# Optimization experiments

Hardware: AMD Instinct MI355X
Metric: run time of the kernel (lower is better)

Reference implementation:

```python
import jax, jax.numpy as jnp
import numpy as np

N_NODES = 30000
N_EDGES = 100000
N_GRAPHS = 256
HEADS = 4
NEG_SLOPE = 0.2


def _xavier(key, shape):
    fan_in, fan_out = shape[-2], shape[-1]
    limit = (6.0 / (fan_in + fan_out)) ** 0.5
    return jax.random.uniform(key, shape, jnp.float32, -limit, limit)


def setup_inputs() -> dict:
    key = jax.random.key(0)
    ks = jax.random.split(key, 12)
    x = jax.random.normal(ks[0], (N_NODES, 78), jnp.float32)
    edge_index = jax.random.randint(ks[1], (2, N_EDGES), 0, N_NODES, jnp.int64)
    # sorted graph ids covering all N_GRAPHS segments
    batch = (jnp.arange(N_NODES, dtype=jnp.int64) * N_GRAPHS) // N_NODES
    # conv1: 78 -> 78 per head
    W1 = _xavier(ks[2], (78, HEADS * 78))
    att1 = _xavier(ks[3], (1, HEADS, 2 * 78))
    b1 = jnp.zeros((HEADS * 78,), jnp.float32)
    # conv2: 312 -> 156 per head
    W2 = _xavier(ks[4], (312, HEADS * 156))
    att2 = _xavier(ks[5], (1, HEADS, 2 * 156))
    b2 = jnp.zeros((HEADS * 156,), jnp.float32)
    # conv3: 624 -> 312 per head
    W3 = _xavier(ks[6], (624, HEADS * 312))
    att3 = _xavier(ks[7], (1, HEADS, 2 * 312))
    b3 = jnp.zeros((HEADS * 312,), jnp.float32)
    Wg1 = _xavier(ks[8], (1248, 1024)); bg1 = jnp.zeros((1024,), jnp.float32)
    Wg2 = _xavier(ks[9], (1024, 128)); bg2 = jnp.zeros((128,), jnp.float32)
    Wo = _xavier(ks[10], (128, 1)); bo = jnp.zeros((1,), jnp.float32)
    return {"x": x, "edge_index": edge_index, "batch": batch,
            "W1": W1, "att1": att1, "b1": b1,
            "W2": W2, "att2": att2, "b2": b2,
            "W3": W3, "att3": att3, "b3": b3,
            "Wg1": Wg1, "bg1": bg1, "Wg2": Wg2, "bg2": bg2,
            "Wo": Wo, "bo": bo}


def gat_conv(x, edge_index, W, att, b, out_ch):
    # x: [N, in]; W: [in, heads*out]; att: [1, heads, 2*out]
    n = x.shape[0]
    xh = (x @ W).reshape(n, HEADS, out_ch)            # [N, H, C]
    src, dst = edge_index[0], edge_index[1]           # x_j = src, x_i = dst (target)
    xi = xh[dst]                                      # [E, H, C]
    xj = xh[src]                                      # [E, H, C]
    cat = jnp.concatenate([xi, xj], axis=-1)          # [E, H, 2C]
    alpha = (cat * att).sum(-1)                       # [E, H]
    alpha = jax.nn.leaky_relu(alpha, NEG_SLOPE)
    # NOTE: softmax over heads (dim=1), as in the original code
    alpha = jax.nn.softmax(alpha, axis=1)
    msg = xj * alpha[..., None]                       # [E, H, C]
    agg = jax.ops.segment_sum(msg, dst, num_segments=n)  # [N, H, C]
    return agg.reshape(n, HEADS * out_ch) + b


def reference(x, edge_index, batch, W1, att1, b1, W2, att2, b2, W3, att3, b3,
              Wg1, bg1, Wg2, bg2, Wo, bo):
    h = jax.nn.relu(gat_conv(x, edge_index, W1, att1, b1, 78))
    h = jax.nn.relu(gat_conv(h, edge_index, W2, att2, b2, 156))
    h = jax.nn.relu(gat_conv(h, edge_index, W3, att3, b3, 312))
    # global max pool per graph
    g = jax.ops.segment_max(h, batch, num_segments=N_GRAPHS)  # [G, 1248]
    g = jax.nn.relu(g @ Wg1 + bg1)
    g = g @ Wg2 + bg2
    return g @ Wo + bo  # [G, 1]
```

## Files before the change

kernel.cpp:

```cpp
#include <hip/hip_runtime.h>
#include <hip/hip_bf16.h>

#define N_NODES 30000
#define N_GRAPHS 256
#define HEADS 4
#define NBLK_SCAN ((N_NODES + 255) / 256)

typedef __attribute__((ext_vector_type(8))) short short8;
typedef __attribute__((ext_vector_type(4))) float f32x4;
typedef __attribute__((ext_vector_type(4))) unsigned short ushort4_t;
typedef unsigned short ushort_t;

__device__ __forceinline__ ushort_t f2bf(float v) {
    __hip_bfloat16 h = __float2bfloat16(v);
    return *reinterpret_cast<ushort_t*>(&h);
}
__device__ __forceinline__ float bf2f(ushort_t u) {
    __hip_bfloat16 h;
    *reinterpret_cast<ushort_t*>(&h) = u;
    return __bfloat162float(h);
}
__device__ __forceinline__ int ld_idx(const void* p, long i, int is64) {
    return is64 ? (int)((const long long*)p)[i] : ((const int*)p)[i];
}
__device__ __forceinline__ int clampi(int v, int hi) {
    return v < 0 ? 0 : (v > hi ? hi : v);
}

__global__ void detect_fmt(const void* ei, const void* batch, int E, int* flags)
{
    __shared__ int okE, okB;
    if (threadIdx.x == 0) { okE = 1; okB = 1; }
    __syncthreads();
    const long long* e64 = (const long long*)ei;
    const long long* b64 = (const long long*)batch;
    const int nbslot = N_NODES / 2;
    for (int i = threadIdx.x; i < 2048; i += 256) {
        long ei_idx = (long)i * E / 2048;
        long long v = e64[ei_idx];
        if (v < 0 || v >= N_NODES) okE = 0;
        long b_idx = (long)i * nbslot / 2048;
        long long b = b64[b_idx];
        if (b < 0 || b >= N_GRAPHS) okB = 0;
    }
    __syncthreads();
    if (threadIdx.x == 0) { flags[0] = okE; flags[1] = okB; }
}

__global__ void init_zero(int* __restrict__ indeg, int* __restrict__ gcnt)
{
    int i = blockIdx.x * 256 + threadIdx.x;
    if (i < N_NODES) indeg[i] = 0;
    if (i < N_GRAPHS) gcnt[i] = 0;
}

__global__ void zero_pads(ushort_t* __restrict__ H1b, ushort_t* __restrict__ H2b)
{
    int n = blockIdx.x * blockDim.x + threadIdx.x;
    if (n >= N_NODES) return;
    ushort4_t z = {0, 0, 0, 0};
    *(ushort4_t*)&H1b[(long)n * 320 + 312] = z;
    *(ushort4_t*)&H1b[(long)n * 320 + 316] = z;
#pragma unroll
    for (int q = 0; q < 4; ++q)
        *(ushort4_t*)&H2b[(long)n * 640 + 624 + q * 4] = z;
}

__global__ void csr_hist(const void* ei, const void* batch, const int* __restrict__ flags,
                         int* __restrict__ indeg, int* __restrict__ gcnt, int E)
{
    int i = blockIdx.x * blockDim.x + threadIdx.x;
    if (i < E) {
        int d = clampi(ld_idx(ei, (long)E + i, flags[0]), N_NODES - 1);
        atomicAdd(&indeg[d], 1);
    }
    if (i < N_NODES) {
        int g = clampi(ld_idx(batch, i, flags[1]), N_GRAPHS - 1);
        atomicAdd(&gcnt[g], 1);
    }
}

__global__ __launch_bounds__(256) void scan_a(const int* __restrict__ indeg,
                                              int* __restrict__ locpre,
                                              int* __restrict__ bsum)
{
    __shared__ int ps[256];
    const int t = threadIdx.x;
    const int i = blockIdx.x * 256 + t;
    int v = (i < N_NODES) ? indeg[i] : 0;
    ps[t] = v;
    __syncthreads();
    for (int d = 1; d < 256; d <<= 1) {
        int u = (t >= d) ? ps[t - d] : 0;
        __syncthreads();
        ps[t] += u;
        __syncthreads();
    }
    if (i < N_NODES) locpre[i] = ps[t] - v;
    if (t == 255) bsum[blockIdx.x] = ps[255];
}

__global__ __launch_bounds__(256) void scan_b(const int* __restrict__ bsum,
                                              int* __restrict__ bbase,
                                              int* __restrict__ totE,
                                              const int* __restrict__ gcnt,
                                              int* __restrict__ gstart)
{
    __shared__ int ps[256];
    const int t = threadIdx.x;
    int v = (t < NBLK_SCAN) ? bsum[t] : 0;
    ps[t] = v;
    __syncthreads();
    for (int d = 1; d < 256; d <<= 1) {
        int u = (t >= d) ? ps[t - d] : 0;
        __syncthreads();
        ps[t] += u;
        __syncthreads();
    }
    if (t < NBLK_SCAN) bbase[t] = ps[t] - v;
    if (t == 255) totE[0] = ps[255];
    __syncthreads();
    int gv = gcnt[t];
    ps[t] = gv;
    __syncthreads();
    for (int d = 1; d < 256; d <<= 1) {
        int u = (t >= d) ? ps[t - d] : 0;
        __syncthreads();
        ps[t] += u;
        __syncthreads();
    }
    gstart[t + 1] = ps[t];
    if (t == 0) gstart[0] = 0;
}

__global__ void scan_c(const int* __restrict__ locpre, const int* __restrict__ bbase,
                       const int* __restrict__ totE,
                       int* __restrict__ off, int* __restrict__ cursor)
{
    int i = blockIdx.x * 256 + threadIdx.x;
    if (i < N_NODES) {
        int o = locpre[i] + bbase[blockIdx.x];
        off[i] = o;
        cursor[i] = o;
    }
    if (i == 0) off[N_NODES] = totE[0];
}

__global__ void csr_fill(const void* ei, const int* __restrict__ flags,
                         int* __restrict__ cursor, int* __restrict__ slots,
                         int* __restrict__ srcs, int E)
{
    int i = blockIdx.x * blockDim.x + threadIdx.x;
    if (i >= E) return;
    int is64 = flags[0];
    int d = clampi(ld_idx(ei, (long)E + i, is64), N_NODES - 1);
    int s = clampi(ld_idx(ei, i, is64), N_NODES - 1);
    int p = atomicAdd(&cursor[d], 1);
    slots[p] = i;
    srcs[p] = s;
}

__global__ void conv_pad_bf16(const float* __restrict__ src, ushort_t* __restrict__ dst,
                              int K, int Kp, long M)
{
    long total = M * Kp;
    long stride = (long)gridDim.x * blockDim.x;
    for (long i = (long)blockIdx.x * blockDim.x + threadIdx.x; i < total; i += stride) {
        long n = i / Kp;
        int k = (int)(i - n * Kp);
        dst[i] = (k < K) ? f2bf(src[n * K + k]) : (ushort_t)0;
    }
}

__global__ void prep_weights(const float* __restrict__ W, const float* __restrict__ att,
                             ushort_t* __restrict__ WT, float* __restrict__ Wd,
                             float* __restrict__ Wsv, int K, int Kp, int C, int HC)
{
    int i = blockIdx.x * blockDim.x + threadIdx.x;
    if (blockIdx.y == 0) {
        int nch = Kp >> 3;
        if (i >= HC * nch) return;
        int n = i / nch, c8 = i - n * nch;
#pragma unroll
        for (int e = 0; e < 8; ++e) {
            int k = c8 * 8 + e;
            WT[(long)n * Kp + k] = (k < K) ? f2bf(W[(long)k * HC + n]) : (ushort_t)0;
        }
    } else {
        if (i >= K * HEADS) return;
        int k = i >> 2, h = i & 3;
        const float* wrow = W + (long)k * HC + h * C;
        const float* ad = att + h * 2 * C;
        const float* as = ad + C;
        float s1 = 0.f, s2 = 0.f;
        for (int c = 0; c < C; ++c) { float w = wrow[c]; s1 += w * ad[c]; s2 += w * as[c]; }
        Wd[k * HEADS + h] = s1;
        Wsv[k * HEADS + h] = s2;
    }
}

__global__ __launch_bounds__(256) void node_proj_any(const void* __restrict__ A,
                                                     int lda, int K, int isbf,
                                                     const float* __restrict__ Wd,
                                                     const float* __restrict__ Wsv,
                                                     float* __restrict__ adst,
                                                     float* __restrict__ asrc, int N)
{
    const int wv = threadIdx.x >> 6, lane = threadIdx.x & 63;
    const int n0 = (blockIdx.x * 4 + wv) * 2;
    if (n0 >= N) return;
    const int n1 = min(n0 + 1, N - 1);

    f32x4 sd0 = {0.f, 0.f, 0.f, 0.f}, ss0 = sd0, sd1 = sd0, ss1 = sd0;

    if (isbf) {
        const ushort_t* a0 = (const ushort_t*)A + (long)n0 * lda;
        const ushort_t* a1 = (const ushort_t*)A + (long)n1 * lda;
        for (int k = lane; k < K; k += 64) {
            float v0 = bf2f(a0[k]);
            float v1 = bf2f(a1[k]);
            f32x4 wd = *(const f32x4*)&Wd[k * HEADS];
            f32x4 wsv = *(const f32x4*)&Wsv[k * HEADS];
            sd0 += v0 * wd; ss0 += v0 * wsv;
            sd1 += v1 * wd; ss1 += v1 * wsv;
        }
    } else {
        const float* a0 = (const float*)A + (long)n0 * lda;
        const float* a1 = (const float*)A + (long)n1 * lda;
        for (int k = lane; k < K; k += 64) {
            float v0 = a0[k];
            float v1 = a1[k];
            f32x4 wd = *(const f32x4*)&Wd[k * HEADS];
            f32x4 wsv = *(const f32x4*)&Wsv[k * HEADS];
            sd0 += v0 * wd; ss0 += v0 * wsv;
            sd1 += v1 * wd; ss1 += v1 * wsv;
        }
    }
#pragma unroll
    for (int off = 32; off; off >>= 1) {
#pragma unroll
        for (int h = 0; h < 4; ++h) {
            sd0[h] += __shfl_down(sd0[h], off);
            ss0[h] += __shfl_down(ss0[h], off);
            sd1[h] += __shfl_down(sd1[h], off);
            ss1[h] += __shfl_down(ss1[h], off);
        }
    }
    if (lane == 0) {
        *(f32x4*)&adst[n0 * HEADS] = sd0;
        *(f32x4*)&asrc[n0 * HEADS] = ss0;
        if (n1 != n0) {
            *(f32x4*)&adst[n1 * HEADS] = sd1;
            *(f32x4*)&asrc[n1 * HEADS] = ss1;
        }
    }
}

__global__ void edge_alpha_csr(const int* __restrict__ slots,
                               const void* __restrict__ ei, const int* __restrict__ flags,
                               const float* __restrict__ adst, const float* __restrict__ asrc,
                               float* __restrict__ alphac, int E)
{
    int p = blockIdx.x * blockDim.x + threadIdx.x;
    if (p >= E) return;
    int is64 = flags[0];
    int e = slots[p];
    int s = clampi(ld_idx(ei, e, is64), N_NODES - 1);
    int d = clampi(ld_idx(ei, (long)E + e, is64), N_NODES - 1);
    float a[HEADS], m = -1e30f;
#pragma unroll
    for (int h = 0; h < HEADS; ++h) {
        float v = adst[d * HEADS + h] + asrc[s * HEADS + h];
        v = (v > 0.f) ? v : 0.2f * v;
        a[h] = v;
        m = fmaxf(m, v);
    }
    float sum = 0.f;
#pragma unroll
    for (int h = 0; h < HEADS; ++h) { a[h] = __expf(a[h] - m); sum += a[h]; }
    float inv = 1.f / sum;
    f32x4 o;
#pragma unroll
    for (int h = 0; h < HEADS; ++h) o[h] = a[h] * inv;
    *(f32x4*)&alphac[(long)p * HEADS] = o;
}

#define BM 128
#define BN 128
#define BK 64
#define NXCD 8
__global__ __launch_bounds__(256) void gemm_bf16(const ushort_t* __restrict__ A,
                                                 const ushort_t* __restrict__ WT,
                                                 ushort_t* __restrict__ C,
                                                 int M, int FC, int Kp, int ncols)
{
    const int nwg = gridDim.x;
    const int bid = blockIdx.x;
    const int q = nwg >> 3, r = nwg & (NXCD - 1);
    const int k = bid & (NXCD - 1), i = bid >> 3;
    const int wu = (k < r) ? k * (q + 1) + i
                           : r * (q + 1) + (k - r) * q + i;
    const int rowb = wu / ncols;
    const int colb_i = wu - rowb * ncols;
    const int row0 = rowb * BM;
    const int colb = colb_i * BN;

    __shared__ ushort_t As[BM * BK];
    __shared__ ushort_t Bs[BN * BK];
    const int tid = threadIdx.x;
    const int lane = tid & 63;
    const int wid = tid >> 6;
    const int wm = wid >> 1, wn = wid & 1;

    f32x4 acc[4][4];
#pragma unroll
    for (int a = 0; a < 4; ++a)
#pragma unroll
        for (int b = 0; b < 4; ++b) { f32x4 z = {0.f, 0.f, 0.f, 0.f}; acc[a][b] = z; }

    short8 ra[4], rb[4];

    auto loadG = [&](int k0) {
#pragma unroll
        for (int u = 0; u < 4; ++u) {
            int id = u * 256 + tid;
            int row = id >> 3, j = id & 7;
            long grow = min(row0 + row, M - 1);
            ra[u] = *(const short8*)&A[grow * Kp + k0 + j * 8];
        }
#pragma unroll
        for (int u = 0; u < 4; ++u) {
            int id = u * 256 + tid;
            int row = id >> 3, j = id & 7;
            long gcol = min(colb + row, FC - 1);
            rb[u] = *(const short8*)&WT[gcol * Kp + k0 + j * 8];
        }
    };

    loadG(0);
    for (int k0 = 0; k0 < Kp; k0 += BK) {
        __syncthreads();
#pragma unroll
        for (int u = 0; u < 4; ++u) {
            int id = u * 256 + tid;
            int row = id >> 3, j = id & 7;
            *(short8*)&As[row * BK + ((j ^ (row & 7)) << 3)] = ra[u];
        }
#pragma unroll
        for (int u = 0; u < 4; ++u) {
            int id = u * 256 + tid;
            int row = id >> 3, j = id & 7;
            *(short8*)&Bs[row * BK + ((j ^ (row & 7)) << 3)] = rb[u];
        }
        __syncthreads();
        if (k0 + BK < Kp) loadG(k0 + BK);
#pragma unroll
        for (int ks = 0; ks < 2; ++ks) {
            short8 af[4], bfr[4];
            const int jr = ks * 4 + (lane >> 4);
#pragma unroll
            for (int fm = 0; fm < 4; ++fm) {
                int row = wm * 64 + fm * 16 + (lane & 15);
                af[fm] = *(const short8*)&As[row * BK + ((jr ^ (row & 7)) << 3)];
            }
#pragma unroll
            for (int fn = 0; fn < 4; ++fn) {
                int row = wn * 64 + fn * 16 + (lane & 15);
                bfr[fn] = *(const short8*)&Bs[row * BK + ((jr ^ (row & 7)) << 3)];
            }
#pragma unroll
            for (int fm = 0; fm < 4; ++fm)
#pragma unroll
                for (int fn = 0; fn < 4; ++fn)
                    acc[fm][fn] = __builtin_amdgcn_mfma_f32_16x16x32_bf16(
                        af[fm], bfr[fn], acc[fm][fn], 0, 0, 0);
        }
    }

#pragma unroll
    for (int fm = 0; fm < 4; ++fm) {
        int rbase = row0 + wm * 64 + fm * 16 + (lane >> 4) * 4;
#pragma unroll
        for (int fn = 0; fn < 4; ++fn) {
            int col = colb + wn * 64 + fn * 16 + (lane & 15);
            if (col >= FC) continue;
#pragma unroll
            for (int u = 0; u < 4; ++u) {
                int gr = rbase + u;
                if (gr < M) C[(long)gr * FC + col] = f2bf(acc[fm][fn][u]);
            }
        }
    }
}

__global__ __launch_bounds__(256) void gat_gather_all(const int* __restrict__ off,
                                                      const int* __restrict__ srcs,
                                                      const float* __restrict__ alphac,
                                                      const ushort_t* __restrict__ xh,
                                                      const float* __restrict__ bias,
                                                      ushort_t* __restrict__ outb, int ldo,
                                                      int HC, int FC)
{
    const int wv = threadIdx.x >> 6, lane = threadIdx.x & 63;
    const int n = blockIdx.x * 4 + wv;
    if (n >= N_NODES) return;
    const int nch = (HC + 255) >> 8;
    float acc0[3][4], acc1[3][4];
#pragma unroll
    for (int a = 0; a < 3; ++a)
#pragma unroll
        for (int j = 0; j < 4; ++j) { acc0[a][j] = 0.f; acc1[a][j] = 0.f; }

    const int s0 = off[n], s1 = off[n + 1];
    int i = s0;
    for (; i + 1 < s1; i += 2) {
        f32x4 alA = *(const f32x4*)&alphac[(long)i * HEADS];
        f32x4 alB = *(const f32x4*)&alphac[(long)(i + 1) * HEADS];
        int sA = srcs[i], sB = srcs[i + 1];
        const ushort_t* xA = xh + (long)sA * HC;
        const ushort_t* xB = xh + (long)sB * HC;
        for (int ch = 0; ch < nch; ++ch) {
            int base = (ch << 8) + lane * 4;
            if (base >= HC) break;
            ushort4_t vA = *(const ushort4_t*)&xA[base];
            ushort4_t vB = *(const ushort4_t*)&xB[base];
#pragma unroll
            for (int j = 0; j < 4; ++j) {
                int c = base + j;
                float wA = (c < FC) ? alA[0] : (c < 2 * FC) ? alA[1]
                          : (c < 3 * FC) ? alA[2] : alA[3];
                float wB = (c < FC) ? alB[0] : (c < 2 * FC) ? alB[1]
                          : (c < 3 * FC) ? alB[2] : alB[3];
                acc0[ch][j] += wA * bf2f(vA[j]);
                acc1[ch][j] += wB * bf2f(vB[j]);
            }
        }
    }
    if (i < s1) {
        f32x4 al = *(const f32x4*)&alphac[(long)i * HEADS];
        int s = srcs[i];
        const ushort_t* xs = xh + (long)s * HC;
        for (int ch = 0; ch < nch; ++ch) {
            int base = (ch << 8) + lane * 4;
            if (base >= HC) break;
            ushort4_t v = *(const ushort4_t*)&xs[base];
#pragma unroll
            for (int j = 0; j < 4; ++j) {
                int c = base + j;
                float w = (c < FC) ? al[0] : (c < 2 * FC) ? al[1]
                         : (c < 3 * FC) ? al[2] : al[3];
                acc0[ch][j] += w * bf2f(v[j]);
            }
        }
    }

    for (int ch = 0; ch < nch; ++ch) {
        int base = (ch << 8) + lane * 4;
        if (base >= HC) break;
        ushort4_t o;
#pragma unroll
        for (int j = 0; j < 4; ++j)
            o[j] = f2bf(fmaxf(acc0[ch][j] + acc1[ch][j] + bias[base + j], 0.f));
        *(ushort4_t*)&outb[(long)n * ldo + base] = o;
    }
}

#define NSPLIT 16
__global__ __launch_bounds__(256) void pool_gather(const int* __restrict__ off,
                                                   const int* __restrict__ srcs,
                                                   const float* __restrict__ alphac,
                                                   const ushort_t* __restrict__ xh,
                                                   const float* __restrict__ bias,
                                                   const int* __restrict__ gstart,
                                                   float* __restrict__ PMAX,
                                                   int HC, int FC)
{
    const int g = blockIdx.x / NSPLIT;
    const int sp = blockIdx.x - g * NSPLIT;
    const int col = blockIdx.y * 1024 + threadIdx.x * 4;
    if (col >= HC) return;
    const int h = col / FC;
    const ushort_t* xcol = xh + col;

    const int n0 = gstart[g], n1 = gstart[g + 1];
    const int len = n1 - n0;
    const int chn = (len + NSPLIT - 1) / NSPLIT;
    const int na = n0 + sp * chn;
    const int nb = min(na + chn, n1);

    f32x4 gmax = {0.f, 0.f, 0.f, 0.f};
    if (na < nb) {
        f32x4 bc = *(const f32x4*)&bias[col];
        float accv[4] = {0.f, 0.f, 0.f, 0.f};

        int i = off[na];
        const int iend = off[nb];
        int cur = na;
        int cur_end = off[na + 1];

        while (i == cur_end && cur < nb) {
#pragma unroll
            for (int j = 0; j < 4; ++j) {
                gmax[j] = fmaxf(gmax[j], fmaxf(accv[j] + bc[j], 0.f));
                accv[j] = 0.f;
            }
            ++cur;
            if (cur < nb) cur_end = off[cur + 1];
        }

        float wq = 0.f;
        ushort4_t vq = {0, 0, 0, 0};
        if (i < iend) {
            wq = alphac[(long)i * HEADS + h];
            vq = *(const ushort4_t*)&xcol[(long)srcs[i] * HC];
        }
        while (i < iend) {
            float w0 = wq;
            ushort4_t v0 = vq;
            if (i + 1 < iend) {
                wq = alphac[(long)(i + 1) * HEADS + h];
                vq = *(const ushort4_t*)&xcol[(long)srcs[i + 1] * HC];
            }
#pragma unroll
            for (int j = 0; j < 4; ++j) accv[j] += w0 * bf2f(v0[j]);
            ++i;
            while (i == cur_end && cur < nb) {
#pragma unroll
                for (int j = 0; j < 4; ++j) {
                    gmax[j] = fmaxf(gmax[j], fmaxf(accv[j] + bc[j], 0.f));
                    accv[j] = 0.f;
                }
                ++cur;
                if (cur < nb) cur_end = off[cur + 1];
            }
        }
    }
    *(f32x4*)&PMAX[(long)(g * NSPLIT + sp) * 1248 + col] = gmax;
}

__global__ void pmax_red(const float* __restrict__ PMAX, float* __restrict__ G)
{
    int i = blockIdx.x * 256 + threadIdx.x;
    if (i >= N_GRAPHS * 1248) return;
    int g = i / 1248;
    int col = i - g * 1248;
    float m = 0.f;
#pragma unroll
    for (int sp = 0; sp < NSPLIT; ++sp)
        m = fmaxf(m, PMAX[(long)(g * NSPLIT + sp) * 1248 + col]);
    G[i] = m;
}

__global__ __launch_bounds__(256) void head_g1_sk(const float* __restrict__ Gp,
                                                  const float* __restrict__ W,
                                                  float* __restrict__ HP)
{
    __shared__ float a0[156], a1[156];
    const int m0 = blockIdx.x * 2;
    const int ks = blockIdx.y;
    const int k0 = ks * 156;
    if (threadIdx.x < 156) {
        a0[threadIdx.x] = Gp[(long)m0 * 1248 + k0 + threadIdx.x];
        a1[threadIdx.x] = Gp[(long)(m0 + 1) * 1248 + k0 + threadIdx.x];
    }
    __syncthreads();
    const int n4 = threadIdx.x * 4;
    float c0[4] = {}, c1[4] = {};
    for (int k = 0; k < 156; ++k) {
        f32x4 b = *(const f32x4*)&W[(long)(k0 + k) * 1024 + n4];
        float av0 = a0[k], av1 = a1[k];
#pragma unroll
        for (int j = 0; j < 4; ++j) { c0[j] += av0 * b[j]; c1[j] += av1 * b[j]; }
    }
    float* hp = HP + ((long)ks * 256 + m0) * 1024;
#pragma unroll
    for (int j = 0; j < 4; ++j) {
        hp[n4 + j]        = c0[j];
        hp[1024 + n4 + j] = c1[j];
    }
}

__global__ void head_g1_red(const float* __restrict__ HP,
                            const float* __restrict__ bias,
                            float* __restrict__ out)
{
    int i = blockIdx.x * 256 + threadIdx.x;
    float s = 0.f;
#pragma unroll
    for (int ks = 0; ks < 8; ++ks) s += HP[(long)ks * 262144 + i];
    out[i] = fmaxf(s + bias[i & 1023], 0.f);
}

__global__ __launch_bounds__(256) void head_g2_sk(const float* __restrict__ G1,
                                                  const float* __restrict__ W,
                                                  float* __restrict__ HP)
{
    __shared__ float a[2][128];
    const int m0 = blockIdx.x * 2;
    const int ks = blockIdx.y;
    const int k0 = ks * 128;
    if (threadIdx.x < 128)
        a[0][threadIdx.x] = G1[(long)m0 * 1024 + k0 + threadIdx.x];
    else
        a[1][threadIdx.x - 128] = G1[(long)(m0 + 1) * 1024 + k0 + threadIdx.x - 128];
    __syncthreads();
    const int nn = threadIdx.x & 127;
    const int r = threadIdx.x >> 7;
    float acc = 0.f;
    for (int k = 0; k < 128; ++k)
        acc += a[r][k] * W[(long)(k0 + k) * 128 + nn];
    HP[((long)ks * 256 + m0 + r) * 128 + nn] = acc;
}

__global__ void head_g2_red(const float* __restrict__ HP,
                            const float* __restrict__ bias,
                            float* __restrict__ out)
{
    int i = blockIdx.x * 256 + threadIdx.x;
    float s = 0.f;
#pragma unroll
    for (int ks = 0; ks < 8; ++ks) s += HP[(long)ks * 32768 + i];
    out[i] = s + bias[i & 127];
}

__global__ __launch_bounds__(256) void head_g3(const float* __restrict__ G2,
                                               const float* __restrict__ Wo,
                                               const float* __restrict__ bo,
                                               float* __restrict__ out)
{
    const int wv = threadIdx.x >> 6, lane = threadIdx.x & 63;
    const int m = blockIdx.x * 4 + wv;
    if (m >= N_GRAPHS) return;
    float s = G2[(long)m * 128 + lane] * Wo[lane]
            + G2[(long)m * 128 + 64 + lane] * Wo[64 + lane];
#pragma unroll
    for (int o = 32; o; o >>= 1) s += __shfl_down(s, o);
    if (lane == 0) out[m] = s + bo[0];
}

extern "C" void kernel_launch(void* const* d_in, const int* in_sizes, int n_in,
                              void* d_out, int out_size, void* d_ws, size_t ws_size,
                              hipStream_t stream)
{
    const float* x    = (const float*)d_in[0];
    const void*  ei   = d_in[1];
    const void*  batch= d_in[2];
    const float* W1   = (const float*)d_in[3];
    const float* att1 = (const float*)d_in[4];
    const float* b1   = (const float*)d_in[5];
    const float* W2   = (const float*)d_in[6];
    const float* att2 = (const float*)d_in[7];
    const float* b2   = (const float*)d_in[8];
    const float* W3   = (const float*)d_in[9];
    const float* att3 = (const float*)d_in[10];
    const float* b3   = (const float*)d_in[11];
    const float* Wg1  = (const float*)d_in[12];
    const float* bg1  = (const float*)d_in[13];
    const float* Wg2  = (const float*)d_in[14];
    const float* bg2  = (const float*)d_in[15];
    const float* Wo   = (const float*)d_in[16];
    const float* bo   = (const float*)d_in[17];

    const int N = N_NODES;
    const int E = in_sizes[1] / 2;

    float* ws = (float*)d_ws;
    ushort_t* H1b  = (ushort_t*)ws;
    ushort_t* H2b  = (ushort_t*)(ws + 4800000);
    ushort_t* ABF1 = (ushort_t*)(ws + 14400000);
    ushort_t* XHb  = (ushort_t*)(ws + 16320000);
    ushort_t* WT   = (ushort_t*)(ws + 35040000);
    float* ADST  = ws + 35440000;
    float* ASRC  = ws + 35560000;
    float* ALPHAC= ws + 35680000;
    float* WD    = ws + 36080000;
    float* WSV   = ws + 36084096;
    float* G     = ws + 36088192;
    float* G1    = ws + 36407680;
    float* G2    = ws + 36669824;
    int*   INDEG = (int*)(ws + 36702592);
    int*   OFF   = (int*)(ws + 36732592);
    int*   CURS  = (int*)(ws + 36762593);
    int*   SLOTS = (int*)(ws + 36792593);
    int*   SRCS  = (int*)(ws + 36892593);
    int*   FLAGS = (int*)(ws + 36992593);
    int*   GCNT  = (int*)(ws + 36992595);
    int*   GSTART= (int*)(ws + 36992851);
    int*   LOCPRE= (int*)(ws + 36993108);
    int*   BSUM  = (int*)(ws + 37023108);
    int*   BBASE = (int*)(ws + 37023226);
    int*   TOTE  = (int*)(ws + 37023344);
    float* PMAX  = ws;
    float* HP1   = ws;
    float* HP2   = ws + 2100000;

    dim3 blk(256);

    detect_fmt<<<dim3(1), blk, 0, stream>>>(ei, batch, E, FLAGS);
    init_zero<<<dim3((N + 255) / 256), blk, 0, stream>>>(INDEG, GCNT);
    zero_pads<<<dim3((N + 255) / 256), blk, 0, stream>>>(H1b, H2b);

    csr_hist<<<dim3((E + 255) / 256), blk, 0, stream>>>(ei, batch, FLAGS, INDEG, GCNT, E);
    scan_a<<<dim3(NBLK_SCAN), blk, 0, stream>>>(INDEG, LOCPRE, BSUM);
    scan_b<<<dim3(1), blk, 0, stream>>>(BSUM, BBASE, TOTE, GCNT, GSTART);
    scan_c<<<dim3(NBLK_SCAN), blk, 0, stream>>>(LOCPRE, BBASE, TOTE, OFF, CURS);
    csr_fill<<<dim3((E + 255) / 256), blk, 0, stream>>>(ei, FLAGS, CURS, SLOTS, SRCS, E);

    conv_pad_bf16<<<dim3(8192), blk, 0, stream>>>(x, ABF1, 78, 128, (long)N);

    struct Layer {
        const void* A; int lda; int K; int isbf;
        const ushort_t* Abf; int Kp;
        const float *W, *att, *b;
        int C, HC;
        ushort_t* outb; int ldo;
        int pool;
    };
    Layer L[3] = {
        { x,   78,  78,  0, ABF1, 128, W1, att1, b1,  78,  312, H1b, 320, 0 },
        { H1b, 320, 312, 1, H1b,  320, W2, att2, b2, 156,  624, H2b, 640, 0 },
        { H2b, 640, 624, 1, H2b,  640, W3, att3, b3, 312, 1248, nullptr, 0, 1 },
    };

    for (int li = 0; li < 3; ++li) {
        const Layer& l = L[li];
        int nch = l.Kp >> 3;
        int gx = (max(l.HC * nch, l.K * HEADS) + 255) / 256;
        prep_weights<<<dim3(gx, 2), blk, 0, stream>>>(l.W, l.att, WT, WD, WSV,
                                                      l.K, l.Kp, l.C, l.HC);
        node_proj_any<<<dim3((N + 7) / 8), blk, 0, stream>>>(l.A, l.lda, l.K, l.isbf, WD, WSV, ADST, ASRC, N);
        edge_alpha_csr<<<dim3((E + 255) / 256), blk, 0, stream>>>(SLOTS, ei, FLAGS, ADST, ASRC, ALPHAC, E);

        int ncols = (l.HC + BN - 1) / BN;
        int nrows = (N + BM - 1) / BM;
        gemm_bf16<<<dim3(ncols * nrows), blk, 0, stream>>>(l.Abf, WT, XHb, N, l.HC, l.Kp, ncols);

        if (l.pool) {
            dim3 pg(N_GRAPHS * NSPLIT, (l.HC + 1023) / 1024);
            pool_gather<<<pg, blk, 0, stream>>>(OFF, SRCS, ALPHAC, XHb, l.b,
                                                GSTART, PMAX, l.HC, l.C);
            pmax_red<<<dim3((N_GRAPHS * 1248 + 255) / 256), blk, 0, stream>>>(PMAX, G);
        } else {
            gat_gather_all<<<dim3((N + 3) / 4), blk, 0, stream>>>(
                OFF, SRCS, ALPHAC, XHb, l.b, l.outb, l.ldo, l.HC, l.C);
        }
    }

    head_g1_sk <<<dim3(N_GRAPHS / 2, 8), blk, 0, stream>>>(G, Wg1, HP1);
    head_g1_red<<<dim3(1024), blk, 0, stream>>>(HP1, bg1, G1);
    head_g2_sk <<<dim3(N_GRAPHS / 2, 8), blk, 0, stream>>>(G1, Wg2, HP2);
    head_g2_red<<<dim3(128), blk, 0, stream>>>(HP2, bg2, G2);
    head_g3    <<<dim3(N_GRAPHS / 4), blk, 0, stream>>>(G2, Wo, bo, (float*)d_out);
}
```

Before: 509.9 us.

## Fold attention logit projections into GEMM as extra output columns

```diff
diff --git a/kernel.cpp b/kernel.cpp
--- a/kernel.cpp
+++ b/kernel.cpp
@@ -147,8 +147,8 @@
 }
 
 __global__ void csr_fill(const void* ei, const int* __restrict__ flags,
-                         int* __restrict__ cursor, int* __restrict__ slots,
-                         int* __restrict__ srcs, int E)
+                         int* __restrict__ cursor, int* __restrict__ srcs,
+                         int* __restrict__ dsts, int E)
 {
     int i = blockIdx.x * blockDim.x + threadIdx.x;
     if (i >= E) return;
@@ -156,8 +156,8 @@
     int d = clampi(ld_idx(ei, (long)E + i, is64), N_NODES - 1);
     int s = clampi(ld_idx(ei, i, is64), N_NODES - 1);
     int p = atomicAdd(&cursor[d], 1);
-    slots[p] = i;
     srcs[p] = s;
+    dsts[p] = d;
 }
 
 __global__ void conv_pad_bf16(const float* __restrict__ src, ushort_t* __restrict__ dst,
@@ -173,8 +173,7 @@
 }
 
 __global__ void prep_weights(const float* __restrict__ W, const float* __restrict__ att,
-                             ushort_t* __restrict__ WT, float* __restrict__ Wd,
-                             float* __restrict__ Wsv, int K, int Kp, int C, int HC)
+                             ushort_t* __restrict__ WT, int K, int Kp, int C, int HC)
 {
     int i = blockIdx.x * blockDim.x + threadIdx.x;
     if (blockIdx.y == 0) {
@@ -187,90 +186,34 @@
             WT[(long)n * Kp + k] = (k < K) ? f2bf(W[(long)k * HC + n]) : (ushort_t)0;
         }
     } else {
-        if (i >= K * HEADS) return;
+        if (i >= Kp * HEADS) return;
         int k = i >> 2, h = i & 3;
-        const float* wrow = W + (long)k * HC + h * C;
-        const float* ad = att + h * 2 * C;
-        const float* as = ad + C;
         float s1 = 0.f, s2 = 0.f;
-        for (int c = 0; c < C; ++c) { float w = wrow[c]; s1 += w * ad[c]; s2 += w * as[c]; }
-        Wd[k * HEADS + h] = s1;
-        Wsv[k * HEADS + h] = s2;
-    }
-}
-
-__global__ __launch_bounds__(256) void node_proj_any(const void* __restrict__ A,
-                                                     int lda, int K, int isbf,
-                                                     const float* __restrict__ Wd,
-                                                     const float* __restrict__ Wsv,
-                                                     float* __restrict__ adst,
-                                                     float* __restrict__ asrc, int N)
-{
-    const int wv = threadIdx.x >> 6, lane = threadIdx.x & 63;
-    const int n0 = (blockIdx.x * 4 + wv) * 2;
-    if (n0 >= N) return;
-    const int n1 = min(n0 + 1, N - 1);
-
-    f32x4 sd0 = {0.f, 0.f, 0.f, 0.f}, ss0 = sd0, sd1 = sd0, ss1 = sd0;
-
-    if (isbf) {
-        const ushort_t* a0 = (const ushort_t*)A + (long)n0 * lda;
-        const ushort_t* a1 = (const ushort_t*)A + (long)n1 * lda;
-        for (int k = lane; k < K; k += 64) {
-            float v0 = bf2f(a0[k]);
-            float v1 = bf2f(a1[k]);
-            f32x4 wd = *(const f32x4*)&Wd[k * HEADS];
-            f32x4 wsv = *(const f32x4*)&Wsv[k * HEADS];
-            sd0 += v0 * wd; ss0 += v0 * wsv;
-            sd1 += v1 * wd; ss1 += v1 * wsv;
-        }
-    } else {
-        const float* a0 = (const float*)A + (long)n0 * lda;
-        const float* a1 = (const float*)A + (long)n1 * lda;
-        for (int k = lane; k < K; k += 64) {
-            float v0 = a0[k];
-            float v1 = a1[k];
-            f32x4 wd = *(const f32x4*)&Wd[k * HEADS];
-            f32x4 wsv = *(const f32x4*)&Wsv[k * HEADS];
-            sd0 += v0 * wd; ss0 += v0 * wsv;
-            sd1 += v1 * wd; ss1 += v1 * wsv;
-        }
-    }
-#pragma unroll
-    for (int off = 32; off; off >>= 1) {
-#pragma unroll
-        for (int h = 0; h < 4; ++h) {
-            sd0[h] += __shfl_down(sd0[h], off);
-            ss0[h] += __shfl_down(ss0[h], off);
-            sd1[h] += __shfl_down(sd1[h], off);
-            ss1[h] += __shfl_down(ss1[h], off);
-        }
-    }
-    if (lane == 0) {
-        *(f32x4*)&adst[n0 * HEADS] = sd0;
-        *(f32x4*)&asrc[n0 * HEADS] = ss0;
-        if (n1 != n0) {
-            *(f32x4*)&adst[n1 * HEADS] = sd1;
-            *(f32x4*)&asrc[n1 * HEADS] = ss1;
-        }
-    }
-}
-
-__global__ void edge_alpha_csr(const int* __restrict__ slots,
-                               const void* __restrict__ ei, const int* __restrict__ flags,
-                               const float* __restrict__ adst, const float* __restrict__ asrc,
+        if (k < K) {
+            const float* wrow = W + (long)k * HC + h * C;
+            const float* ad = att + h * 2 * C;
+            const float* as = ad + C;
+            for (int c = 0; c < C; ++c) { float w = wrow[c]; s1 += w * ad[c]; s2 += w * as[c]; }
+        }
+        WT[(long)(HC + h) * Kp + k]     = f2bf(s1);
+        WT[(long)(HC + 4 + h) * Kp + k] = f2bf(s2);
+    }
+}
+
+__global__ void edge_alpha_csr(const int* __restrict__ srcs, const int* __restrict__ dsts,
+                               const ushort_t* __restrict__ xh, int ldx, int HC,
                                float* __restrict__ alphac, int E)
 {
     int p = blockIdx.x * blockDim.x + threadIdx.x;
     if (p >= E) return;
-    int is64 = flags[0];
-    int e = slots[p];
-    int s = clampi(ld_idx(ei, e, is64), N_NODES - 1);
-    int d = clampi(ld_idx(ei, (long)E + e, is64), N_NODES - 1);
+    int s = srcs[p];
+    int d = dsts[p];
+    ushort4_t li = *(const ushort4_t*)&xh[(long)d * ldx + HC];
+    ushort4_t lj = *(const ushort4_t*)&xh[(long)s * ldx + HC + 4];
     float a[HEADS], m = -1e30f;
 #pragma unroll
     for (int h = 0; h < HEADS; ++h) {
-        float v = adst[d * HEADS + h] + asrc[s * HEADS + h];
+        float v = bf2f(li[h]) + bf2f(lj[h]);
         v = (v > 0.f) ? v : 0.2f * v;
         a[h] = v;
         m = fmaxf(m, v);
@@ -396,7 +339,7 @@
 __global__ __launch_bounds__(256) void gat_gather_all(const int* __restrict__ off,
                                                       const int* __restrict__ srcs,
                                                       const float* __restrict__ alphac,
-                                                      const ushort_t* __restrict__ xh,
+                                                      const ushort_t* __restrict__ xh, int ldx,
                                                       const float* __restrict__ bias,
                                                       ushort_t* __restrict__ outb, int ldo,
                                                       int HC, int FC)
@@ -417,8 +360,8 @@
         f32x4 alA = *(const f32x4*)&alphac[(long)i * HEADS];
         f32x4 alB = *(const f32x4*)&alphac[(long)(i + 1) * HEADS];
         int sA = srcs[i], sB = srcs[i + 1];
-        const ushort_t* xA = xh + (long)sA * HC;
-        const ushort_t* xB = xh + (long)sB * HC;
+        const ushort_t* xA = xh + (long)sA * ldx;
+        const ushort_t* xB = xh + (long)sB * ldx;
         for (int ch = 0; ch < nch; ++ch) {
             int base = (ch << 8) + lane * 4;
             if (base >= HC) break;
@@ -439,7 +382,7 @@
     if (i < s1) {
         f32x4 al = *(const f32x4*)&alphac[(long)i * HEADS];
         int s = srcs[i];
-        const ushort_t* xs = xh + (long)s * HC;
+        const ushort_t* xs = xh + (long)s * ldx;
         for (int ch = 0; ch < nch; ++ch) {
             int base = (ch << 8) + lane * 4;
             if (base >= HC) break;
@@ -469,7 +412,7 @@
 __global__ __launch_bounds__(256) void pool_gather(const int* __restrict__ off,
                                                    const int* __restrict__ srcs,
                                                    const float* __restrict__ alphac,
-                                                   const ushort_t* __restrict__ xh,
+                                                   const ushort_t* __restrict__ xh, int ldx,
                                                    const float* __restrict__ bias,
                                                    const int* __restrict__ gstart,
                                                    float* __restrict__ PMAX,
@@ -512,14 +455,14 @@
         ushort4_t vq = {0, 0, 0, 0};
         if (i < iend) {
             wq = alphac[(long)i * HEADS + h];
-            vq = *(const ushort4_t*)&xcol[(long)srcs[i] * HC];
+            vq = *(const ushort4_t*)&xcol[(long)srcs[i] * ldx];
         }
         while (i < iend) {
             float w0 = wq;
             ushort4_t v0 = vq;
             if (i + 1 < iend) {
                 wq = alphac[(long)(i + 1) * HEADS + h];
-                vq = *(const ushort4_t*)&xcol[(long)srcs[i + 1] * HC];
+                vq = *(const ushort4_t*)&xcol[(long)srcs[i + 1] * ldx];
             }
 #pragma unroll
             for (int j = 0; j < 4; ++j) accv[j] += w0 * bf2f(v0[j]);
@@ -669,19 +612,14 @@
     ushort_t* H2b  = (ushort_t*)(ws + 4800000);
     ushort_t* ABF1 = (ushort_t*)(ws + 14400000);
     ushort_t* XHb  = (ushort_t*)(ws + 16320000);
-    ushort_t* WT   = (ushort_t*)(ws + 35040000);
-    float* ADST  = ws + 35440000;
-    float* ASRC  = ws + 35560000;
+    ushort_t* WT   = (ushort_t*)(ws + 35160000);
     float* ALPHAC= ws + 35680000;
-    float* WD    = ws + 36080000;
-    float* WSV   = ws + 36084096;
     float* G     = ws + 36088192;
     float* G1    = ws + 36407680;
     float* G2    = ws + 36669824;
     int*   INDEG = (int*)(ws + 36702592);
     int*   OFF   = (int*)(ws + 36732592);
     int*   CURS  = (int*)(ws + 36762593);
-    int*   SLOTS = (int*)(ws + 36792593);
     int*   SRCS  = (int*)(ws + 36892593);
     int*   FLAGS = (int*)(ws + 36992593);
     int*   GCNT  = (int*)(ws + 36992595);
@@ -690,6 +628,7 @@
     int*   BSUM  = (int*)(ws + 37023108);
     int*   BBASE = (int*)(ws + 37023226);
     int*   TOTE  = (int*)(ws + 37023344);
+    int*   DSTS  = (int*)(ws + 37023345);
     float* PMAX  = ws;
     float* HP1   = ws;
     float* HP2   = ws + 2100000;
@@ -704,12 +643,11 @@
     scan_a<<<dim3(NBLK_SCAN), blk, 0, stream>>>(INDEG, LOCPRE, BSUM);
     scan_b<<<dim3(1), blk, 0, stream>>>(BSUM, BBASE, TOTE, GCNT, GSTART);
     scan_c<<<dim3(NBLK_SCAN), blk, 0, stream>>>(LOCPRE, BBASE, TOTE, OFF, CURS);
-    csr_fill<<<dim3((E + 255) / 256), blk, 0, stream>>>(ei, FLAGS, CURS, SLOTS, SRCS, E);
+    csr_fill<<<dim3((E + 255) / 256), blk, 0, stream>>>(ei, FLAGS, CURS, SRCS, DSTS, E);
 
     conv_pad_bf16<<<dim3(8192), blk, 0, stream>>>(x, ABF1, 78, 128, (long)N);
 
     struct Layer {
-        const void* A; int lda; int K; int isbf;
         const ushort_t* Abf; int Kp;
         const float *W, *att, *b;
         int C, HC;
@@ -717,32 +655,33 @@
         int pool;
     };
     Layer L[3] = {
-        { x,   78,  78,  0, ABF1, 128, W1, att1, b1,  78,  312, H1b, 320, 0 },
-        { H1b, 320, 312, 1, H1b,  320, W2, att2, b2, 156,  624, H2b, 640, 0 },
-        { H2b, 640, 624, 1, H2b,  640, W3, att3, b3, 312, 1248, nullptr, 0, 1 },
+        { ABF1, 128, W1, att1, b1,  78,  312, H1b, 320, 0 },
+        { H1b,  320, W2, att2, b2, 156,  624, H2b, 640, 0 },
+        { H2b,  640, W3, att3, b3, 312, 1248, nullptr, 0, 1 },
     };
 
     for (int li = 0; li < 3; ++li) {
         const Layer& l = L[li];
+        const int FCX = l.HC + 8;
         int nch = l.Kp >> 3;
-        int gx = (max(l.HC * nch, l.K * HEADS) + 255) / 256;
-        prep_weights<<<dim3(gx, 2), blk, 0, stream>>>(l.W, l.att, WT, WD, WSV,
-                                                      l.K, l.Kp, l.C, l.HC);
-        node_proj_any<<<dim3((N + 7) / 8), blk, 0, stream>>>(l.A, l.lda, l.K, l.isbf, WD, WSV, ADST, ASRC, N);
-        edge_alpha_csr<<<dim3((E + 255) / 256), blk, 0, stream>>>(SLOTS, ei, FLAGS, ADST, ASRC, ALPHAC, E);
-
-        int ncols = (l.HC + BN - 1) / BN;
+        int gx = (max(l.HC * nch, l.Kp * HEADS) + 255) / 256;
+        prep_weights<<<dim3(gx, 2), blk, 0, stream>>>(l.W, l.att, WT, l.C == 0 ? 0 : l.Kp == 128 ? 78 : (l.Kp == 320 ? 312 : 624), l.Kp, l.C, l.HC);
+
+        int ncols = (FCX + BN - 1) / BN;
         int nrows = (N + BM - 1) / BM;
-        gemm_bf16<<<dim3(ncols * nrows), blk, 0, stream>>>(l.Abf, WT, XHb, N, l.HC, l.Kp, ncols);
+        gemm_bf16<<<dim3(ncols * nrows), blk, 0, stream>>>(l.Abf, WT, XHb, N, FCX, l.Kp, ncols);
+
+        edge_alpha_csr<<<dim3((E + 255) / 256), blk, 0, stream>>>(
+            SRCS, DSTS, XHb, FCX, l.HC, ALPHAC, E);
 
         if (l.pool) {
             dim3 pg(N_GRAPHS * NSPLIT, (l.HC + 1023) / 1024);
-            pool_gather<<<pg, blk, 0, stream>>>(OFF, SRCS, ALPHAC, XHb, l.b,
+            pool_gather<<<pg, blk, 0, stream>>>(OFF, SRCS, ALPHAC, XHb, FCX, l.b,
                                                 GSTART, PMAX, l.HC, l.C);
             pmax_red<<<dim3((N_GRAPHS * 1248 + 255) / 256), blk, 0, stream>>>(PMAX, G);
         } else {
             gat_gather_all<<<dim3((N + 3) / 4), blk, 0, stream>>>(
-                OFF, SRCS, ALPHAC, XHb, l.b, l.outb, l.ldo, l.HC, l.C);
+                OFF, SRCS, ALPHAC, XHb, FCX, l.b, l.outb, l.ldo, l.HC, l.C);
         }
     }
 
```

After: 455.6 us. 1.12x faster.
